# Kernel optimization log

Hardware: AMD Instinct MI355X
Metric: run time of the kernel (lower is better)

## Reference

```python
import jax, jax.numpy as jnp
import numpy as np

B, S, D, H = 2, 2048, 1024, 16
DK = D // H
NEG = -1.0e9


def setup_inputs() -> dict:
    key = jax.random.key(0)
    ks = jax.random.split(key, 11)
    inp = {
        "q": jax.random.normal(ks[0], (B, S, D), jnp.float32),
        "k": jax.random.normal(ks[1], (B, S, D), jnp.float32),
        "v": jax.random.normal(ks[2], (B, S, D), jnp.float32),
        "mask": jnp.tril(jnp.ones((S, S), jnp.int32))[None, None],  # causal [1,1,S,S]
    }
    scale = 0.02
    inp["w_q"] = jax.random.normal(ks[3], (D, D), jnp.float32) * scale
    inp["b_q"] = jnp.zeros((D,), jnp.float32)
    inp["w_k"] = jax.random.normal(ks[4], (D, D), jnp.float32) * scale
    inp["b_k"] = jnp.zeros((D,), jnp.float32)
    inp["w_v"] = jax.random.normal(ks[5], (D, D), jnp.float32) * scale
    inp["b_v"] = jnp.zeros((D,), jnp.float32)
    inp["w_o"] = jax.random.normal(ks[6], (D, D), jnp.float32) * scale
    inp["b_o"] = jnp.zeros((D,), jnp.float32)
    return inp


def reference(q, k, v, mask, w_q, b_q, w_k, b_k, w_v, b_v, w_o, b_o):
    # projections: [B,S,D] -> [B,H,S,DK]
    def proj(x, w, b):
        y = jnp.einsum("bsd,de->bse", x, w) + b
        return y.reshape(B, S, H, DK).transpose(0, 2, 1, 3)

    Q = proj(q, w_q, b_q)
    K = proj(k, w_k, b_k)
    V = proj(v, w_v, b_v)
    # explicit scores matrix, faithful to the original naive attention
    scores = jnp.einsum("bhsd,bhtd->bhst", Q, K) / jnp.sqrt(jnp.float32(DK))
    scores = jnp.where(mask == 0, NEG, scores)
    attn = jax.nn.softmax(scores, axis=-1)  # dropout p=0.0 -> identity
    x = jnp.einsum("bhst,bhtd->bhsd", attn, V)
    x = x.transpose(0, 2, 1, 3).reshape(B, S, D)
    return jnp.einsum("bsd,de->bse", x, w_o) + b_o
```

## Files before the change

kernel.cpp:

```cpp
#include <hip/hip_runtime.h>
#include <hip/hip_bf16.h>

typedef __bf16 bf16;
typedef __bf16 bf16x2 __attribute__((ext_vector_type(2)));
typedef __bf16 bf16x8 __attribute__((ext_vector_type(8)));
typedef float f32x4 __attribute__((ext_vector_type(4)));

#define MFMA16(a, b, c) __builtin_amdgcn_mfma_f32_16x16x32_bf16(a, b, c, 0, 0, 0)

#define QSCALE 0.18033688f

__global__ __launch_bounds__(256) void convert_k(const float* __restrict__ q,
                                                 const float* __restrict__ k,
                                                 const float* __restrict__ v,
                                                 bf16* __restrict__ qb,
                                                 bf16* __restrict__ kb,
                                                 bf16* __restrict__ vb) {
  const float* src = blockIdx.y == 0 ? q : blockIdx.y == 1 ? k : v;
  bf16* dst = blockIdx.y == 0 ? qb : blockIdx.y == 1 ? kb : vb;
  const size_t i = ((size_t)blockIdx.x * 256 + threadIdx.x) * 8;
  float4 a = *(const float4*)(src + i);
  float4 b = *(const float4*)(src + i + 4);
  bf16x8 o;
  o[0] = (bf16)a.x; o[1] = (bf16)a.y; o[2] = (bf16)a.z; o[3] = (bf16)a.w;
  o[4] = (bf16)b.x; o[5] = (bf16)b.y; o[6] = (bf16)b.z; o[7] = (bf16)b.w;
  *(bf16x8*)(dst + i) = o;
}

__global__ __launch_bounds__(256) void transpose_w(const float* __restrict__ w0,
                                                   const float* __restrict__ w1,
                                                   const float* __restrict__ w2,
                                                   const float* __restrict__ w3,
                                                   bf16* __restrict__ dst) {
  __shared__ bf16 T[64][68];
  const float* W = blockIdx.z == 0 ? w0 : blockIdx.z == 1 ? w1
                   : blockIdx.z == 2 ? w2 : w3;
  bf16* Y = dst + (size_t)blockIdx.z * 1024 * 1024;
  const int t = threadIdx.x, r = t >> 2, c4 = t & 3;
  const int k0 = blockIdx.y * 64, n0 = blockIdx.x * 64;

  const float4* src = (const float4*)(W + (size_t)(k0 + r) * 1024 + n0 + c4 * 16);
  float4 f0 = src[0], f1 = src[1], f2 = src[2], f3 = src[3];
  bf16* row = &T[r][c4 * 16];
  row[0] = (bf16)f0.x; row[1] = (bf16)f0.y; row[2] = (bf16)f0.z; row[3] = (bf16)f0.w;
  row[4] = (bf16)f1.x; row[5] = (bf16)f1.y; row[6] = (bf16)f1.z; row[7] = (bf16)f1.w;
  row[8] = (bf16)f2.x; row[9] = (bf16)f2.y; row[10] = (bf16)f2.z; row[11] = (bf16)f2.w;
  row[12] = (bf16)f3.x; row[13] = (bf16)f3.y; row[14] = (bf16)f3.z; row[15] = (bf16)f3.w;
  __syncthreads();

  bf16x8 o0, o1;
#pragma unroll
  for (int j = 0; j < 8; ++j) o0[j] = T[c4 * 16 + j][r];
#pragma unroll
  for (int j = 0; j < 8; ++j) o1[j] = T[c4 * 16 + 8 + j][r];
  bf16* d = Y + (size_t)(n0 + r) * 1024 + k0 + c4 * 16;
  *(bf16x8*)d = o0;
  *(bf16x8*)(d + 8) = o1;
}

template <int QKV, int MT>
__global__ __launch_bounds__(256, 3) void gemm_p(
    const bf16* __restrict__ xq, const bf16* __restrict__ xk,
    const bf16* __restrict__ xv, const bf16* __restrict__ Wt,
    const float* __restrict__ bq, const float* __restrict__ bk,
    const float* __restrict__ bv, bf16* __restrict__ Qp,
    bf16* __restrict__ Kp, bf16* __restrict__ Vtp, float* __restrict__ Yf) {
  constexpr int AROWS = MT * 32;
  __shared__ bf16 Al[AROWS * 72];
  __shared__ bf16 Bl[128 * 72];

  const int z = QKV ? blockIdx.z : 0;
  const bf16* X = QKV ? (z == 0 ? xq : z == 1 ? xk : xv) : xq;
  const bf16* Bt = Wt + (size_t)z * 1048576;
  const float* bias = QKV ? (z == 0 ? bq : z == 1 ? bk : bv) : bq;
  const float escale = (QKV && z == 0) ? QSCALE : 1.0f;

  const int t = threadIdx.x;
  const int wave = t >> 6, lane = t & 63, quad = lane >> 4, l16 = lane & 15;
  const int wm = (wave >> 1) * (MT * 16), wn = (wave & 1) * 64;
  const int bm = blockIdx.y * AROWS, bn = blockIdx.x * 128;

  constexpr int NA = (MT == 4) ? 4 : 2;
  const int arow = (MT == 4) ? (t >> 1) : (t >> 2);
  const int acol = (MT == 4) ? ((t & 1) * 32) : ((t & 3) * 16);
  const int brow = t >> 1, bcol = (t & 1) * 32;
  const bf16* gA = X + (size_t)(bm + arow) * 1024 + acol;
  const bf16* gB = Bt + (size_t)(bn + brow) * 1024 + bcol;

  bf16x8 ra[NA], rb[4];
#pragma unroll
  for (int j = 0; j < NA; ++j) ra[j] = *(const bf16x8*)(gA + j * 8);
#pragma unroll
  for (int j = 0; j < 4; ++j) rb[j] = *(const bf16x8*)(gB + j * 8);

  f32x4 acc[MT][4] = {};

  for (int kb = 0; kb < 1024; kb += 64) {
    __syncthreads();
#pragma unroll
    for (int j = 0; j < NA; ++j)
      *(bf16x8*)(Al + arow * 72 + acol + j * 8) = ra[j];
#pragma unroll
    for (int j = 0; j < 4; ++j)
      *(bf16x8*)(Bl + brow * 72 + bcol + j * 8) = rb[j];
    __syncthreads();

    if (kb + 64 < 1024) {
#pragma unroll
      for (int j = 0; j < NA; ++j)
        ra[j] = *(const bf16x8*)(gA + kb + 64 + j * 8);
#pragma unroll
      for (int j = 0; j < 4; ++j)
        rb[j] = *(const bf16x8*)(gB + kb + 64 + j * 8);
    }

#pragma unroll
    for (int kk = 0; kk < 2; ++kk) {
      bf16x8 af[MT], bfr[4];
#pragma unroll
      for (int mt = 0; mt < MT; ++mt)
        af[mt] =
            *(const bf16x8*)(Al + (wm + mt * 16 + l16) * 72 + kk * 32 + quad * 8);
#pragma unroll
      for (int nt = 0; nt < 4; ++nt)
        bfr[nt] =
            *(const bf16x8*)(Bl + (wn + nt * 16 + l16) * 72 + kk * 32 + quad * 8);
#pragma unroll
      for (int mt = 0; mt < MT; ++mt)
#pragma unroll
        for (int nt = 0; nt < 4; ++nt)
          acc[mt][nt] = MFMA16(af[mt], bfr[nt], acc[mt][nt]);
    }
  }

  if (QKV && z == 2) {
    bf16* Tt = Al;
    const int b = bm >> 11;
    __syncthreads();
#pragma unroll
    for (int half = 0; half < 2; ++half) {
      if ((wave & 1) == half) {
#pragma unroll
        for (int nt = 0; nt < 4; ++nt) {
          const int ln = nt * 16 + l16;
          const float bia = bias[bn + half * 64 + ln];
#pragma unroll
          for (int mt = 0; mt < 4; ++mt)
#pragma unroll
            for (int r = 0; r < 4; ++r) {
              const int m = wm + mt * 16 + quad * 4 + r;
              Tt[ln * 136 + m] = (bf16)(acc[mt][nt][r] + bia);
            }
        }
      }
      __syncthreads();
      {
        const int ln = t >> 2, seg = (t & 3) * 32;
        const int gn = bn + half * 64 + ln;
        const int h = gn >> 6, dk = gn & 63;
        const int s0 = (bm & 2047) + seg;
        bf16* dstp = Vtp + ((size_t)(b * 16 + h) * 64 + dk) * 2048 + s0;
        const bf16* srcp = Tt + ln * 136 + seg;
#pragma unroll
        for (int j = 0; j < 4; ++j)
          *(bf16x8*)(dstp + j * 8) = *(const bf16x8*)(srcp + j * 8);
      }
      __syncthreads();
    }
  } else {
#pragma unroll
    for (int mt = 0; mt < MT; ++mt)
#pragma unroll
      for (int nt = 0; nt < 4; ++nt) {
        const int gn = bn + wn + nt * 16 + l16;
        const float bia = bias[gn];
#pragma unroll
        for (int r = 0; r < 4; ++r) {
          const int gm = bm + wm + mt * 16 + quad * 4 + r;
          const float val = (acc[mt][nt][r] + bia) * escale;
          if (!QKV) {
            Yf[(size_t)gm * 1024 + gn] = val;
          } else {
            const int b = gm >> 11, s = gm & 2047;
            const int h = gn >> 6, dk = gn & 63;
            bf16* Y = (z == 0) ? Qp : Kp;
            Y[((size_t)(b * 16 + h) * 2048 + s) * 64 + dk] = (bf16)val;
          }
        }
      }
  }
}

__global__ __launch_bounds__(256) void attn_k(const bf16* __restrict__ Q,
                                              const bf16* __restrict__ K,
                                              const bf16* __restrict__ Vt,
                                              bf16* __restrict__ X) {
  __shared__ bf16 Kl[64 * 72];
  __shared__ bf16 Vl[64 * 72];
  __shared__ bf16 Pb[4][16 * 72];

  const int t = threadIdx.x;
  const int wave = t >> 6, lane = t & 63, quad = lane >> 4, l16 = lane & 15;
  const int pairx = blockIdx.x, bh = blockIdx.y;
  const int b = bh >> 4, h = bh & 15;

  const bf16* Qb = Q + (size_t)bh * 2048 * 64;
  const bf16* Kb = K + (size_t)bh * 2048 * 64;
  const bf16* Vb = Vt + (size_t)bh * 64 * 2048;

  const int srow = t >> 2;
  const int scol = (t & 3) * 16;
  const int crow = (srow & 32) + ((srow & 1) << 4) + ((srow & 31) >> 1);

  bf16x8 onesf;
#pragma unroll
  for (int i = 0; i < 8; ++i) onesf[i] = (bf16)1.0f;

  bf16* Pw = Pb[wave];

  for (int phase = 0; phase < 2; ++phase) {
    const int qtile = phase ? (31 - pairx) : pairx;
    const int ntiles = qtile + 1;
    const int q0 = qtile * 64 + wave * 16;

    bf16x8 qf0 = *(const bf16x8*)(Qb + (q0 + l16) * 64 + quad * 8);
    bf16x8 qf1 = *(const bf16x8*)(Qb + (q0 + l16) * 64 + 32 + quad * 8);

    f32x4 o[4] = {};
    f32x4 o4 = {};

    {
      const bf16* kp = Kb + srow * 64 + scol;
      const bf16* vp = Vb + (size_t)srow * 2048 + scol;
      bf16x8 k0r = *(const bf16x8*)kp;
      bf16x8 k1r = *(const bf16x8*)(kp + 8);
      bf16x8 v0r = *(const bf16x8*)vp;
      bf16x8 v1r = *(const bf16x8*)(vp + 8);
      *(bf16x8*)(Kl + crow * 72 + scol) = k0r;
      *(bf16x8*)(Kl + crow * 72 + scol + 8) = k1r;
      *(bf16x8*)(Vl + srow * 72 + scol) = v0r;
      *(bf16x8*)(Vl + srow * 72 + scol + 8) = v1r;
    }
    __syncthreads();

    for (int kt = 0; kt < ntiles; ++kt) {
      const int k0 = kt * 64;
      const bool more = (kt + 1) < ntiles;
      bf16x8 kr0, kr1, vr0, vr1;
      if (more) {
        const bf16* kp = Kb + (k0 + 64 + srow) * 64 + scol;
        const bf16* vp = Vb + (size_t)srow * 2048 + k0 + 64 + scol;
        kr0 = *(const bf16x8*)kp;
        kr1 = *(const bf16x8*)(kp + 8);
        vr0 = *(const bf16x8*)vp;
        vr1 = *(const bf16x8*)(vp + 8);
      }

      f32x4 sc[4];
#pragma unroll
      for (int nt = 0; nt < 4; ++nt) {
        bf16x8 kf0 = *(const bf16x8*)(Kl + (nt * 16 + l16) * 72 + quad * 8);
        bf16x8 kf1 = *(const bf16x8*)(Kl + (nt * 16 + l16) * 72 + 32 + quad * 8);
        f32x4 s = {};
        s = MFMA16(qf0, kf0, s);
        s = MFMA16(qf1, kf1, s);
        sc[nt] = s;
      }

      const bool interior = (k0 + 63) <= q0;
#pragma unroll
      for (int r = 0; r < 4; ++r) {
        const int row = quad * 4 + r;
        float e0 = exp2f(sc[0][r]);
        float e1 = exp2f(sc[1][r]);
        float e2 = exp2f(sc[2][r]);
        float e3 = exp2f(sc[3][r]);
        if (!interior) {
          const int qg = q0 + row;
          const int key0 = k0 + 2 * l16;
          if (key0 > qg) e0 = 0.f;
          if (key0 + 1 > qg) e1 = 0.f;
          if (key0 + 32 > qg) e2 = 0.f;
          if (key0 + 33 > qg) e3 = 0.f;
        }
        bf16x2 p01, p23;
        p01[0] = (bf16)e0; p01[1] = (bf16)e1;
        p23[0] = (bf16)e2; p23[1] = (bf16)e3;
        *(bf16x2*)(Pw + row * 72 + 2 * l16) = p01;
        *(bf16x2*)(Pw + row * 72 + 32 + 2 * l16) = p23;
      }
      __builtin_amdgcn_s_waitcnt(0xC07F);

      bf16x8 pf0 = *(const bf16x8*)(Pw + l16 * 72 + quad * 8);
      bf16x8 pf1 = *(const bf16x8*)(Pw + l16 * 72 + 32 + quad * 8);
      o4 = MFMA16(pf0, onesf, o4);
      o4 = MFMA16(pf1, onesf, o4);
#pragma unroll
      for (int dt = 0; dt < 4; ++dt) {
        bf16x8 vf0 = *(const bf16x8*)(Vl + (dt * 16 + l16) * 72 + quad * 8);
        bf16x8 vf1 = *(const bf16x8*)(Vl + (dt * 16 + l16) * 72 + 32 + quad * 8);
        o[dt] = MFMA16(pf0, vf0, o[dt]);
        o[dt] = MFMA16(pf1, vf1, o[dt]);
      }

      __syncthreads();
      if (more) {
        *(bf16x8*)(Kl + crow * 72 + scol) = kr0;
        *(bf16x8*)(Kl + crow * 72 + scol + 8) = kr1;
        *(bf16x8*)(Vl + srow * 72 + scol) = vr0;
        *(bf16x8*)(Vl + srow * 72 + scol + 8) = vr1;
        __syncthreads();
      }
    }

#pragma unroll
    for (int r = 0; r < 4; ++r) {
      const float rinv = 1.0f / o4[r];
      const int qg = q0 + quad * 4 + r;
#pragma unroll
      for (int dt = 0; dt < 4; ++dt) {
        const int col = h * 64 + dt * 16 + l16;
        X[((size_t)b * 2048 + qg) * 1024 + col] = (bf16)(o[dt][r] * rinv);
      }
    }
    __syncthreads();
  }
}

extern "C" void kernel_launch(void* const* d_in, const int* in_sizes, int n_in,
                              void* d_out, int out_size, void* d_ws,
                              size_t ws_size, hipStream_t stream) {
  const float* q = (const float*)d_in[0];
  const float* k = (const float*)d_in[1];
  const float* v = (const float*)d_in[2];
  const float* w_q = (const float*)d_in[4];
  const float* b_q = (const float*)d_in[5];
  const float* w_k = (const float*)d_in[6];
  const float* b_k = (const float*)d_in[7];
  const float* w_v = (const float*)d_in[8];
  const float* b_v = (const float*)d_in[9];
  const float* w_o = (const float*)d_in[10];
  const float* b_o = (const float*)d_in[11];

  bf16* ws = (bf16*)d_ws;
  const size_t NELEM = (size_t)4096 * 1024;
  bf16* Qp = ws;
  bf16* Kp = ws + NELEM;
  bf16* Vtp = ws + 2 * NELEM;
  bf16* Xp = ws + 3 * NELEM;
  bf16* Wt = ws + 4 * NELEM;
  bf16* Wto = Wt + 3145728;
  bf16* qb = Xp;
  bf16* kb = (bf16*)d_out;
  bf16* vb = kb + NELEM;

  convert_k<<<dim3(2048, 3), 256, 0, stream>>>(q, k, v, qb, kb, vb);
  transpose_w<<<dim3(16, 16, 4), 256, 0, stream>>>(w_q, w_k, w_v, w_o, Wt);

  gemm_p<1, 4><<<dim3(8, 32, 3), 256, 0, stream>>>(
      qb, kb, vb, Wt, b_q, b_k, b_v, Qp, Kp, Vtp, nullptr);
  attn_k<<<dim3(16, 32), 256, 0, stream>>>(Qp, Kp, Vtp, Xp);
  gemm_p<0, 2><<<dim3(8, 64), 256, 0, stream>>>(
      Xp, nullptr, nullptr, Wto, b_o, nullptr, nullptr, nullptr, nullptr,
      nullptr, (float*)d_out);
}
```

Baseline: 243.9 us.

## Fuse fp32-to-bf16 input conversion into QKV GEMM and interleave paired attention tiles

Drops the separate convert kernel: the QKV projection GEMM now loads fp32 activations directly and converts them to bf16 while staging into LDS. The attention kernel processes its low and high causal query tiles together in one pass over K/V, so each K/V tile is loaded once and shared by both, instead of running the two tiles as separate phases. The grid axes are also swapped so that consecutive blocks share weight columns or the same head. The cost is higher register pressure from the fp32 prefetch buffers and the doubled attention accumulators, plus a second P buffer in shared memory.

```diff
diff --git a/kernel.cpp b/kernel.cpp
--- a/kernel.cpp
+++ b/kernel.cpp
@@ -9,23 +9,6 @@
 #define MFMA16(a, b, c) __builtin_amdgcn_mfma_f32_16x16x32_bf16(a, b, c, 0, 0, 0)
 
 #define QSCALE 0.18033688f
-
-__global__ __launch_bounds__(256) void convert_k(const float* __restrict__ q,
-                                                 const float* __restrict__ k,
-                                                 const float* __restrict__ v,
-                                                 bf16* __restrict__ qb,
-                                                 bf16* __restrict__ kb,
-                                                 bf16* __restrict__ vb) {
-  const float* src = blockIdx.y == 0 ? q : blockIdx.y == 1 ? k : v;
-  bf16* dst = blockIdx.y == 0 ? qb : blockIdx.y == 1 ? kb : vb;
-  const size_t i = ((size_t)blockIdx.x * 256 + threadIdx.x) * 8;
-  float4 a = *(const float4*)(src + i);
-  float4 b = *(const float4*)(src + i + 4);
-  bf16x8 o;
-  o[0] = (bf16)a.x; o[1] = (bf16)a.y; o[2] = (bf16)a.z; o[3] = (bf16)a.w;
-  o[4] = (bf16)b.x; o[5] = (bf16)b.y; o[6] = (bf16)b.z; o[7] = (bf16)b.w;
-  *(bf16x8*)(dst + i) = o;
-}
 
 __global__ __launch_bounds__(256) void transpose_w(const float* __restrict__ w0,
                                                    const float* __restrict__ w1,
@@ -60,55 +43,82 @@
 
 template <int QKV, int MT>
 __global__ __launch_bounds__(256, 3) void gemm_p(
-    const bf16* __restrict__ xq, const bf16* __restrict__ xk,
-    const bf16* __restrict__ xv, const bf16* __restrict__ Wt,
-    const float* __restrict__ bq, const float* __restrict__ bk,
-    const float* __restrict__ bv, bf16* __restrict__ Qp,
+    const void* __restrict__ x0, const void* __restrict__ x1,
+    const void* __restrict__ x2, const bf16* __restrict__ Wt,
+    const float* __restrict__ b0, const float* __restrict__ b1,
+    const float* __restrict__ b2, bf16* __restrict__ Qp,
     bf16* __restrict__ Kp, bf16* __restrict__ Vtp, float* __restrict__ Yf) {
   constexpr int AROWS = MT * 32;
   __shared__ bf16 Al[AROWS * 72];
   __shared__ bf16 Bl[128 * 72];
 
   const int z = QKV ? blockIdx.z : 0;
-  const bf16* X = QKV ? (z == 0 ? xq : z == 1 ? xk : xv) : xq;
   const bf16* Bt = Wt + (size_t)z * 1048576;
-  const float* bias = QKV ? (z == 0 ? bq : z == 1 ? bk : bv) : bq;
+  const float* bias = QKV ? (z == 0 ? b0 : z == 1 ? b1 : b2) : b0;
   const float escale = (QKV && z == 0) ? QSCALE : 1.0f;
 
   const int t = threadIdx.x;
   const int wave = t >> 6, lane = t & 63, quad = lane >> 4, l16 = lane & 15;
   const int wm = (wave >> 1) * (MT * 16), wn = (wave & 1) * 64;
-  const int bm = blockIdx.y * AROWS, bn = blockIdx.x * 128;
-
-  constexpr int NA = (MT == 4) ? 4 : 2;
+  const int bm = blockIdx.x * AROWS, bn = blockIdx.y * 128;
+
+  const int brow = t >> 1, bcol = (t & 1) * 32;
+  const bf16* gB = Bt + (size_t)(bn + brow) * 1024 + bcol;
+  bf16x8 rb[4];
+#pragma unroll
+  for (int j = 0; j < 4; ++j) rb[j] = *(const bf16x8*)(gB + j * 8);
+
   const int arow = (MT == 4) ? (t >> 1) : (t >> 2);
   const int acol = (MT == 4) ? ((t & 1) * 32) : ((t & 3) * 16);
-  const int brow = t >> 1, bcol = (t & 1) * 32;
-  const bf16* gA = X + (size_t)(bm + arow) * 1024 + acol;
-  const bf16* gB = Bt + (size_t)(bn + brow) * 1024 + bcol;
-
-  bf16x8 ra[NA], rb[4];
-#pragma unroll
-  for (int j = 0; j < NA; ++j) ra[j] = *(const bf16x8*)(gA + j * 8);
-#pragma unroll
-  for (int j = 0; j < 4; ++j) rb[j] = *(const bf16x8*)(gB + j * 8);
+  const float* gAf = nullptr;
+  const bf16* gAb = nullptr;
+  float4 raf[8];
+  bf16x8 rab[2];
+  if (QKV) {
+    const float* Xf = z == 0 ? (const float*)x0
+                      : z == 1 ? (const float*)x1 : (const float*)x2;
+    gAf = Xf + (size_t)(bm + arow) * 1024 + acol;
+#pragma unroll
+    for (int j = 0; j < 8; ++j) raf[j] = ((const float4*)gAf)[j];
+  } else {
+    gAb = (const bf16*)x0 + (size_t)(bm + arow) * 1024 + acol;
+#pragma unroll
+    for (int j = 0; j < 2; ++j) rab[j] = *(const bf16x8*)(gAb + j * 8);
+  }
 
   f32x4 acc[MT][4] = {};
 
   for (int kb = 0; kb < 1024; kb += 64) {
     __syncthreads();
-#pragma unroll
-    for (int j = 0; j < NA; ++j)
-      *(bf16x8*)(Al + arow * 72 + acol + j * 8) = ra[j];
+    if (QKV) {
+#pragma unroll
+      for (int j = 0; j < 4; ++j) {
+        float4 a = raf[2 * j], b = raf[2 * j + 1];
+        bf16x8 w;
+        w[0] = (bf16)a.x; w[1] = (bf16)a.y; w[2] = (bf16)a.z; w[3] = (bf16)a.w;
+        w[4] = (bf16)b.x; w[5] = (bf16)b.y; w[6] = (bf16)b.z; w[7] = (bf16)b.w;
+        *(bf16x8*)(Al + arow * 72 + acol + j * 8) = w;
+      }
+    } else {
+#pragma unroll
+      for (int j = 0; j < 2; ++j)
+        *(bf16x8*)(Al + arow * 72 + acol + j * 8) = rab[j];
+    }
 #pragma unroll
     for (int j = 0; j < 4; ++j)
       *(bf16x8*)(Bl + brow * 72 + bcol + j * 8) = rb[j];
     __syncthreads();
 
     if (kb + 64 < 1024) {
-#pragma unroll
-      for (int j = 0; j < NA; ++j)
-        ra[j] = *(const bf16x8*)(gA + kb + 64 + j * 8);
+      if (QKV) {
+#pragma unroll
+        for (int j = 0; j < 8; ++j)
+          raf[j] = ((const float4*)(gAf + kb + 64))[j];
+      } else {
+#pragma unroll
+        for (int j = 0; j < 2; ++j)
+          rab[j] = *(const bf16x8*)(gAb + kb + 64 + j * 8);
+      }
 #pragma unroll
       for (int j = 0; j < 4; ++j)
         rb[j] = *(const bf16x8*)(gB + kb + 64 + j * 8);
@@ -197,11 +207,12 @@
                                               bf16* __restrict__ X) {
   __shared__ bf16 Kl[64 * 72];
   __shared__ bf16 Vl[64 * 72];
-  __shared__ bf16 Pb[4][16 * 72];
+  __shared__ bf16 PbL[4][16 * 72];
+  __shared__ bf16 PbH[4][16 * 72];
 
   const int t = threadIdx.x;
   const int wave = t >> 6, lane = t & 63, quad = lane >> 4, l16 = lane & 15;
-  const int pairx = blockIdx.x, bh = blockIdx.y;
+  const int bh = blockIdx.x, pairx = blockIdx.y;
   const int b = bh >> 4, h = bh & 15;
 
   const bf16* Qb = Q + (size_t)bh * 2048 * 64;
@@ -216,68 +227,75 @@
 #pragma unroll
   for (int i = 0; i < 8; ++i) onesf[i] = (bf16)1.0f;
 
-  bf16* Pw = Pb[wave];
-
-  for (int phase = 0; phase < 2; ++phase) {
-    const int qtile = phase ? (31 - pairx) : pairx;
-    const int ntiles = qtile + 1;
-    const int q0 = qtile * 64 + wave * 16;
-
-    bf16x8 qf0 = *(const bf16x8*)(Qb + (q0 + l16) * 64 + quad * 8);
-    bf16x8 qf1 = *(const bf16x8*)(Qb + (q0 + l16) * 64 + 32 + quad * 8);
-
-    f32x4 o[4] = {};
-    f32x4 o4 = {};
+  bf16* PwL = PbL[wave];
+  bf16* PwH = PbH[wave];
+
+  const int qtL = pairx, qtH = 31 - pairx;
+  const int ntiles = qtH + 1;
+  const int q0L = qtL * 64 + wave * 16, q0H = qtH * 64 + wave * 16;
+
+  bf16x8 qfL0 = *(const bf16x8*)(Qb + (q0L + l16) * 64 + quad * 8);
+  bf16x8 qfL1 = *(const bf16x8*)(Qb + (q0L + l16) * 64 + 32 + quad * 8);
+  bf16x8 qfH0 = *(const bf16x8*)(Qb + (q0H + l16) * 64 + quad * 8);
+  bf16x8 qfH1 = *(const bf16x8*)(Qb + (q0H + l16) * 64 + 32 + quad * 8);
+
+  f32x4 oL[4] = {}, oH[4] = {};
+  f32x4 o4L = {}, o4H = {};
+
+  {
+    const bf16* kp = Kb + srow * 64 + scol;
+    const bf16* vp = Vb + (size_t)srow * 2048 + scol;
+    bf16x8 k0r = *(const bf16x8*)kp;
+    bf16x8 k1r = *(const bf16x8*)(kp + 8);
+    bf16x8 v0r = *(const bf16x8*)vp;
+    bf16x8 v1r = *(const bf16x8*)(vp + 8);
+    *(bf16x8*)(Kl + crow * 72 + scol) = k0r;
+    *(bf16x8*)(Kl + crow * 72 + scol + 8) = k1r;
+    *(bf16x8*)(Vl + srow * 72 + scol) = v0r;
+    *(bf16x8*)(Vl + srow * 72 + scol + 8) = v1r;
+  }
+  __syncthreads();
+
+  for (int kt = 0; kt < ntiles; ++kt) {
+    const int k0 = kt * 64;
+    const bool more = (kt + 1) < ntiles;
+    const bool loAct = (kt <= qtL);
+    bf16x8 kr0, kr1, vr0, vr1;
+    if (more) {
+      const bf16* kp = Kb + (k0 + 64 + srow) * 64 + scol;
+      const bf16* vp = Vb + (size_t)srow * 2048 + k0 + 64 + scol;
+      kr0 = *(const bf16x8*)kp;
+      kr1 = *(const bf16x8*)(kp + 8);
+      vr0 = *(const bf16x8*)vp;
+      vr1 = *(const bf16x8*)(vp + 8);
+    }
+
+    f32x4 scH[4], scL[4];
+#pragma unroll
+    for (int nt = 0; nt < 4; ++nt) {
+      bf16x8 kf0 = *(const bf16x8*)(Kl + (nt * 16 + l16) * 72 + quad * 8);
+      bf16x8 kf1 = *(const bf16x8*)(Kl + (nt * 16 + l16) * 72 + 32 + quad * 8);
+      f32x4 s = {};
+      s = MFMA16(qfH0, kf0, s);
+      s = MFMA16(qfH1, kf1, s);
+      scH[nt] = s;
+      if (loAct) {
+        f32x4 s2 = {};
+        s2 = MFMA16(qfL0, kf0, s2);
+        s2 = MFMA16(qfL1, kf1, s2);
+        scL[nt] = s2;
+      }
+    }
 
     {
-      const bf16* kp = Kb + srow * 64 + scol;
-      const bf16* vp = Vb + (size_t)srow * 2048 + scol;
-      bf16x8 k0r = *(const bf16x8*)kp;
-      bf16x8 k1r = *(const bf16x8*)(kp + 8);
-      bf16x8 v0r = *(const bf16x8*)vp;
-      bf16x8 v1r = *(const bf16x8*)(vp + 8);
-      *(bf16x8*)(Kl + crow * 72 + scol) = k0r;
-      *(bf16x8*)(Kl + crow * 72 + scol + 8) = k1r;
-      *(bf16x8*)(Vl + srow * 72 + scol) = v0r;
-      *(bf16x8*)(Vl + srow * 72 + scol + 8) = v1r;
-    }
-    __syncthreads();
-
-    for (int kt = 0; kt < ntiles; ++kt) {
-      const int k0 = kt * 64;
-      const bool more = (kt + 1) < ntiles;
-      bf16x8 kr0, kr1, vr0, vr1;
-      if (more) {
-        const bf16* kp = Kb + (k0 + 64 + srow) * 64 + scol;
-        const bf16* vp = Vb + (size_t)srow * 2048 + k0 + 64 + scol;
-        kr0 = *(const bf16x8*)kp;
-        kr1 = *(const bf16x8*)(kp + 8);
-        vr0 = *(const bf16x8*)vp;
-        vr1 = *(const bf16x8*)(vp + 8);
-      }
-
-      f32x4 sc[4];
-#pragma unroll
-      for (int nt = 0; nt < 4; ++nt) {
-        bf16x8 kf0 = *(const bf16x8*)(Kl + (nt * 16 + l16) * 72 + quad * 8);
-        bf16x8 kf1 = *(const bf16x8*)(Kl + (nt * 16 + l16) * 72 + 32 + quad * 8);
-        f32x4 s = {};
-        s = MFMA16(qf0, kf0, s);
-        s = MFMA16(qf1, kf1, s);
-        sc[nt] = s;
-      }
-
-      const bool interior = (k0 + 63) <= q0;
+      const bool interiorH = (k0 + 63) <= q0H;
 #pragma unroll
       for (int r = 0; r < 4; ++r) {
         const int row = quad * 4 + r;
-        float e0 = exp2f(sc[0][r]);
-        float e1 = exp2f(sc[1][r]);
-        float e2 = exp2f(sc[2][r]);
-        float e3 = exp2f(sc[3][r]);
-        if (!interior) {
-          const int qg = q0 + row;
-          const int key0 = k0 + 2 * l16;
+        float e0 = exp2f(scH[0][r]), e1 = exp2f(scH[1][r]);
+        float e2 = exp2f(scH[2][r]), e3 = exp2f(scH[3][r]);
+        if (!interiorH) {
+          const int qg = q0H + row, key0 = k0 + 2 * l16;
           if (key0 > qg) e0 = 0.f;
           if (key0 + 1 > qg) e1 = 0.f;
           if (key0 + 32 > qg) e2 = 0.f;
@@ -286,44 +304,78 @@
         bf16x2 p01, p23;
         p01[0] = (bf16)e0; p01[1] = (bf16)e1;
         p23[0] = (bf16)e2; p23[1] = (bf16)e3;
-        *(bf16x2*)(Pw + row * 72 + 2 * l16) = p01;
-        *(bf16x2*)(Pw + row * 72 + 32 + 2 * l16) = p23;
-      }
-      __builtin_amdgcn_s_waitcnt(0xC07F);
-
-      bf16x8 pf0 = *(const bf16x8*)(Pw + l16 * 72 + quad * 8);
-      bf16x8 pf1 = *(const bf16x8*)(Pw + l16 * 72 + 32 + quad * 8);
-      o4 = MFMA16(pf0, onesf, o4);
-      o4 = MFMA16(pf1, onesf, o4);
-#pragma unroll
-      for (int dt = 0; dt < 4; ++dt) {
-        bf16x8 vf0 = *(const bf16x8*)(Vl + (dt * 16 + l16) * 72 + quad * 8);
-        bf16x8 vf1 = *(const bf16x8*)(Vl + (dt * 16 + l16) * 72 + 32 + quad * 8);
-        o[dt] = MFMA16(pf0, vf0, o[dt]);
-        o[dt] = MFMA16(pf1, vf1, o[dt]);
-      }
-
+        *(bf16x2*)(PwH + row * 72 + 2 * l16) = p01;
+        *(bf16x2*)(PwH + row * 72 + 32 + 2 * l16) = p23;
+      }
+    }
+    if (loAct) {
+      const bool interiorL = (k0 + 63) <= q0L;
+#pragma unroll
+      for (int r = 0; r < 4; ++r) {
+        const int row = quad * 4 + r;
+        float e0 = exp2f(scL[0][r]), e1 = exp2f(scL[1][r]);
+        float e2 = exp2f(scL[2][r]), e3 = exp2f(scL[3][r]);
+        if (!interiorL) {
+          const int qg = q0L + row, key0 = k0 + 2 * l16;
+          if (key0 > qg) e0 = 0.f;
+          if (key0 + 1 > qg) e1 = 0.f;
+          if (key0 + 32 > qg) e2 = 0.f;
+          if (key0 + 33 > qg) e3 = 0.f;
+        }
+        bf16x2 p01, p23;
+        p01[0] = (bf16)e0; p01[1] = (bf16)e1;
+        p23[0] = (bf16)e2; p23[1] = (bf16)e3;
+        *(bf16x2*)(PwL + row * 72 + 2 * l16) = p01;
+        *(bf16x2*)(PwL + row * 72 + 32 + 2 * l16) = p23;
+      }
+    }
+    __builtin_amdgcn_s_waitcnt(0xC07F);
+
+    bf16x8 pH0 = *(const bf16x8*)(PwH + l16 * 72 + quad * 8);
+    bf16x8 pH1 = *(const bf16x8*)(PwH + l16 * 72 + 32 + quad * 8);
+    o4H = MFMA16(pH0, onesf, o4H);
+    o4H = MFMA16(pH1, onesf, o4H);
+    bf16x8 pL0, pL1;
+    if (loAct) {
+      pL0 = *(const bf16x8*)(PwL + l16 * 72 + quad * 8);
+      pL1 = *(const bf16x8*)(PwL + l16 * 72 + 32 + quad * 8);
+      o4L = MFMA16(pL0, onesf, o4L);
+      o4L = MFMA16(pL1, onesf, o4L);
+    }
+#pragma unroll
+    for (int dt = 0; dt < 4; ++dt) {
+      bf16x8 vf0 = *(const bf16x8*)(Vl + (dt * 16 + l16) * 72 + quad * 8);
+      bf16x8 vf1 = *(const bf16x8*)(Vl + (dt * 16 + l16) * 72 + 32 + quad * 8);
+      oH[dt] = MFMA16(pH0, vf0, oH[dt]);
+      oH[dt] = MFMA16(pH1, vf1, oH[dt]);
+      if (loAct) {
+        oL[dt] = MFMA16(pL0, vf0, oL[dt]);
+        oL[dt] = MFMA16(pL1, vf1, oL[dt]);
+      }
+    }
+
+    __syncthreads();
+    if (more) {
+      *(bf16x8*)(Kl + crow * 72 + scol) = kr0;
+      *(bf16x8*)(Kl + crow * 72 + scol + 8) = kr1;
+      *(bf16x8*)(Vl + srow * 72 + scol) = vr0;
+      *(bf16x8*)(Vl + srow * 72 + scol + 8) = vr1;
       __syncthreads();
-      if (more) {
-        *(bf16x8*)(Kl + crow * 72 + scol) = kr0;
-        *(bf16x8*)(Kl + crow * 72 + scol + 8) = kr1;
-        *(bf16x8*)(Vl + srow * 72 + scol) = vr0;
-        *(bf16x8*)(Vl + srow * 72 + scol + 8) = vr1;
-        __syncthreads();
-      }
-    }
-
-#pragma unroll
-    for (int r = 0; r < 4; ++r) {
-      const float rinv = 1.0f / o4[r];
-      const int qg = q0 + quad * 4 + r;
-#pragma unroll
-      for (int dt = 0; dt < 4; ++dt) {
-        const int col = h * 64 + dt * 16 + l16;
-        X[((size_t)b * 2048 + qg) * 1024 + col] = (bf16)(o[dt][r] * rinv);
-      }
-    }
-    __syncthreads();
+    }
+  }
+
+#pragma unroll
+  for (int r = 0; r < 4; ++r) {
+    const float rinvL = 1.0f / o4L[r];
+    const float rinvH = 1.0f / o4H[r];
+    const int qgL = q0L + quad * 4 + r;
+    const int qgH = q0H + quad * 4 + r;
+#pragma unroll
+    for (int dt = 0; dt < 4; ++dt) {
+      const int col = h * 64 + dt * 16 + l16;
+      X[((size_t)b * 2048 + qgL) * 1024 + col] = (bf16)(oL[dt][r] * rinvL);
+      X[((size_t)b * 2048 + qgH) * 1024 + col] = (bf16)(oH[dt][r] * rinvH);
+    }
   }
 }
 
@@ -350,17 +402,13 @@
   bf16* Xp = ws + 3 * NELEM;
   bf16* Wt = ws + 4 * NELEM;
   bf16* Wto = Wt + 3145728;
-  bf16* qb = Xp;
-  bf16* kb = (bf16*)d_out;
-  bf16* vb = kb + NELEM;
-
-  convert_k<<<dim3(2048, 3), 256, 0, stream>>>(q, k, v, qb, kb, vb);
+
   transpose_w<<<dim3(16, 16, 4), 256, 0, stream>>>(w_q, w_k, w_v, w_o, Wt);
 
-  gemm_p<1, 4><<<dim3(8, 32, 3), 256, 0, stream>>>(
-      qb, kb, vb, Wt, b_q, b_k, b_v, Qp, Kp, Vtp, nullptr);
-  attn_k<<<dim3(16, 32), 256, 0, stream>>>(Qp, Kp, Vtp, Xp);
-  gemm_p<0, 2><<<dim3(8, 64), 256, 0, stream>>>(
+  gemm_p<1, 4><<<dim3(32, 8, 3), 256, 0, stream>>>(
+      q, k, v, Wt, b_q, b_k, b_v, Qp, Kp, Vtp, nullptr);
+  attn_k<<<dim3(32, 16), 256, 0, stream>>>(Qp, Kp, Vtp, Xp);
+  gemm_p<0, 2><<<dim3(64, 8), 256, 0, stream>>>(
       Xp, nullptr, nullptr, Wto, b_o, nullptr, nullptr, nullptr, nullptr,
       nullptr, (float*)d_out);
 }
```

After: 263.1 us. +7.9%, slower.
